# Kernel tuning notes

Measured on AMD Instinct MI355X. Metric: run time of the kernel, lower is better.

## Reference

```python
import jax, jax.numpy as jnp
import numpy as np

IMAGE_SIZE = 224
FMAP_H = FMAP_W = 26   # resnet18 layer2 (28x28) after AvgPool2d(3, stride=1)
N_REWEIGHT = 3
SIGMA = 4.0
KSIZE = 2 * int(4.0 * SIGMA + 0.5) + 1  # 33, kornia-style default kernel for sigma=4


def _gaussian_kernel1d():
    x = np.arange(KSIZE, dtype=np.float64) - (KSIZE - 1) / 2.0
    k = np.exp(-0.5 * (x / SIGMA) ** 2)
    return jnp.asarray((k / k.sum()).astype(np.float32))


def _cdist(x, y):
    # Euclidean cdist: x [N,D], y [M,D] -> [N,M], via the expanded quadratic form.
    x2 = jnp.sum(x * x, axis=1, keepdims=True)          # [N,1]
    y2 = jnp.sum(y * y, axis=1)                          # [M]
    d2 = x2 + y2 - 2.0 * (x @ y.T)                       # [N,M]
    return jnp.sqrt(jnp.maximum(d2, 0.0))


def _gaussian_blur(img):
    # Separable depthwise gaussian blur with reflect padding, img [1,1,H,W].
    k1d = _gaussian_kernel1d()
    pad = (KSIZE - 1) // 2
    x = jnp.pad(img, ((0, 0), (0, 0), (pad, pad), (pad, pad)), mode='reflect')
    kh = k1d.reshape(1, 1, KSIZE, 1)
    kw = k1d.reshape(1, 1, 1, KSIZE)
    dn = ('NCHW', 'OIHW', 'NCHW')
    x = jax.lax.conv_general_dilated(x, kh, (1, 1), 'VALID', dimension_numbers=dn)
    x = jax.lax.conv_general_dilated(x, kw, (1, 1), 'VALID', dimension_numbers=dn)
    return x


def setup_inputs() -> dict:
    key = jax.random.key(0)
    k1, k2 = jax.random.split(key)
    patch = jax.random.normal(k1, (FMAP_H * FMAP_W, 384), dtype=jnp.float32)      # [676, 384]
    patch_lib = jax.random.normal(k2, (100000, 384), dtype=jnp.float32)            # coreset bank
    return {"patch": patch, "patch_lib": patch_lib}


def reference(patch, patch_lib):
    # dist = torch.cdist(patch, patch_lib); min over memory bank
    dist = _cdist(patch, patch_lib)                      # [N, M]
    min_val = jnp.min(dist, axis=1)                      # [N]
    min_idx = jnp.argmin(dist, axis=1)                   # [N]
    s_idx = jnp.argmax(min_val)                          # most anomalous patch
    s_star = min_val[s_idx]
    m_test = patch[s_idx]                                # [D]
    m_star = patch_lib[min_idx[s_idx]]                   # [D]
    # reweighting: k nearest neighbors of m_star in the bank (smallest distances)
    w_dist = jnp.linalg.norm(m_star[None, :] - patch_lib, axis=1)   # [M]
    _, nn_idx = jax.lax.top_k(-w_dist, N_REWEIGHT)                  # indices of k smallest
    m_star_knn = jnp.linalg.norm(m_test[None, :] - patch_lib[nn_idx[1:]], axis=1)  # [k-1]
    D = jnp.sqrt(jnp.asarray(patch.shape[1], dtype=jnp.float32))
    w = 1.0 - jnp.exp(s_star / D) / jnp.sum(jnp.exp(m_star_knn / D))
    s = w * s_star
    # segmentation map: reshape, bilinear upsample (align_corners=False), gaussian blur
    s_map = min_val.reshape(1, 1, FMAP_H, FMAP_W)
    s_map = jax.image.resize(s_map, (1, 1, IMAGE_SIZE, IMAGE_SIZE), method='bilinear')
    s_map = _gaussian_blur(s_map)
    return s, s_map
```

## Files before the change

### kernel.cpp

```cpp
#include <hip/hip_runtime.h>

#define M_PATCH 676
#define K_DIM   384
#define N_LIB   100000
#define BM      128
#define BN      128
#define BK      32
#define LDT     40
#define NCH     782
#define MTILES  6
#define M_PAD   (MTILES*BM)
#define N_PAD   (NCH*BN)
#define NTOPB   1563
#define NCAND   (NTOPB*3)
#define IMG     224
#define FMAP    26
#define KS      33
#define KHALF   16

typedef __attribute__((ext_vector_type(4))) float  f32x4;
typedef __attribute__((ext_vector_type(8))) short  short8;
typedef unsigned long long ull;

static __device__ __forceinline__ unsigned short f2bf(float f) {
  unsigned u = __float_as_uint(f);
  u = u + 0x7FFFu + ((u >> 16) & 1u);
  return (unsigned short)(u >> 16);
}

static __device__ __forceinline__ ull shfl_xor_u64(ull v, int m) {
  unsigned lo = (unsigned)v, hi = (unsigned)(v >> 32);
  lo = __shfl_xor(lo, m, 64);
  hi = __shfl_xor(hi, m, 64);
  return ((ull)hi << 32) | lo;
}

static __device__ __forceinline__ ull umin64(ull a, ull b) { return a < b ? a : b; }
static __device__ __forceinline__ ull umax64(ull a, ull b) { return a > b ? a : b; }

static __device__ __forceinline__ void gld16(const unsigned short* g, unsigned short* l) {
  __builtin_amdgcn_global_load_lds(
      (const __attribute__((address_space(1))) void*)g,
      (__attribute__((address_space(3))) void*)l, 16, 0, 0);
}

__global__ void pc_norms_cvt_kernel(const float* __restrict__ patch, const float* __restrict__ lib,
                                    float* __restrict__ y2, float* __restrict__ x2,
                                    unsigned short* __restrict__ Abf, unsigned short* __restrict__ Bbf,
                                    int do_cvt) {
  const int w = threadIdx.x >> 6, lane = threadIdx.x & 63;
  const long r = (long)blockIdx.x * 4 + w;
  if (r < N_PAD) {
    float s;
    if (r < N_LIB) {
      const float* p = lib + r * K_DIM;
      float v[6];
      s = 0.f;
      #pragma unroll
      for (int j = 0; j < 6; ++j) { v[j] = p[lane + 64 * j]; s += v[j] * v[j]; }
      if (do_cvt) {
        #pragma unroll
        for (int j = 0; j < 6; ++j) Bbf[r * K_DIM + lane + 64 * j] = f2bf(v[j]);
      }
      #pragma unroll
      for (int m = 1; m < 64; m <<= 1) s += __shfl_xor(s, m, 64);
    } else {
      s = __builtin_inff();
      if (do_cvt) {
        #pragma unroll
        for (int j = 0; j < 6; ++j) Bbf[r * K_DIM + lane + 64 * j] = 0;
      }
    }
    if (lane == 0) y2[r] = s;
  } else {
    const long pr = r - N_PAD;
    if (pr < M_PATCH) {
      const float* p = patch + pr * K_DIM;
      float v[6]; float s = 0.f;
      #pragma unroll
      for (int j = 0; j < 6; ++j) { v[j] = p[lane + 64 * j]; s += v[j] * v[j]; }
      if (do_cvt) {
        #pragma unroll
        for (int j = 0; j < 6; ++j) Abf[pr * K_DIM + lane + 64 * j] = f2bf(v[j]);
      }
      #pragma unroll
      for (int m = 1; m < 64; m <<= 1) s += __shfl_xor(s, m, 64);
      if (lane == 0) x2[pr] = s;
    } else if (pr < M_PAD) {
      if (do_cvt) {
        #pragma unroll
        for (int j = 0; j < 6; ++j) Abf[pr * K_DIM + lane + 64 * j] = 0;
      }
    }
  }
}

__launch_bounds__(256, 4)
__global__ void pc_gemm_min_bf16_kernel(const unsigned short* __restrict__ Abf,
                                        const unsigned short* __restrict__ Bbf,
                                        const float* __restrict__ x2g, const float* __restrict__ y2g,
                                        ull* __restrict__ partial) {
  __shared__ unsigned short As[BM * 32];
  __shared__ unsigned short Bs[BN * 32];
  __shared__ float x2s[BM];
  __shared__ float y2s[BN];
  __shared__ ull red[BM * 2];

  const int t = threadIdx.x;
  const int m0 = blockIdx.x * BM;
  const int n0 = blockIdx.y * BN;
  const int wid = t >> 6, lane = t & 63;

  if (t < BM) {
    const int gm = m0 + t;
    x2s[t] = (gm < M_PATCH) ? x2g[gm] : 0.f;
    y2s[t] = y2g[n0 + t];
  }

  const int srow   = (wid << 4) + (lane >> 2);
  const int spiece = (lane & 3) ^ ((lane >> 4) & 3);
  const unsigned short* gA0 = Abf + (size_t)(m0 + srow) * K_DIM + spiece * 8;
  const unsigned short* gA1 = gA0 + (size_t)64 * K_DIM;
  const unsigned short* gB0 = Bbf + (size_t)(n0 + srow) * K_DIM + spiece * 8;
  const unsigned short* gB1 = gB0 + (size_t)64 * K_DIM;
  unsigned short* lA0 = &As[wid * 512];
  unsigned short* lA1 = &As[(wid + 4) * 512];
  unsigned short* lB0 = &Bs[wid * 512];
  unsigned short* lB1 = &Bs[(wid + 4) * 512];

  f32x4 acc[4][4];
  #pragma unroll
  for (int i = 0; i < 4; ++i)
    #pragma unroll
    for (int j = 0; j < 4; ++j) acc[i][j] = (f32x4){0.f, 0.f, 0.f, 0.f};

  const int wm = wid >> 1, wn = wid & 1;
  const int quad = lane >> 4, l15 = lane & 15;
  const int poff = (quad ^ ((l15 >> 2) & 3)) * 8;

  for (int ks = 0; ks < K_DIM / BK; ++ks) {
    __syncthreads();
    gld16(gA0 + ks * BK, lA0);
    gld16(gA1 + ks * BK, lA1);
    gld16(gB0 + ks * BK, lB0);
    gld16(gB1 + ks * BK, lB1);
    __builtin_amdgcn_s_waitcnt(0);
    __syncthreads();

    short8 af[4], bf[4];
    #pragma unroll
    for (int mi = 0; mi < 4; ++mi)
      af[mi] = *(const short8*)&As[(wm * 64 + mi * 16 + l15) * 32 + poff];
    #pragma unroll
    for (int ni = 0; ni < 4; ++ni)
      bf[ni] = *(const short8*)&Bs[(wn * 64 + ni * 16 + l15) * 32 + poff];

    #pragma unroll
    for (int mi = 0; mi < 4; ++mi)
      #pragma unroll
      for (int ni = 0; ni < 4; ++ni)
        acc[mi][ni] = __builtin_amdgcn_mfma_f32_16x16x32_bf16(af[mi], bf[ni], acc[mi][ni], 0, 0, 0);
  }

  #pragma unroll
  for (int mi = 0; mi < 4; ++mi) {
    #pragma unroll
    for (int r = 0; r < 4; ++r) {
      const int row_l = wm * 64 + mi * 16 + quad * 4 + r;
      const float xs = x2s[row_l];
      ull kmin = ~0ull;
      #pragma unroll
      for (int ni = 0; ni < 4; ++ni) {
        const int col_l = wn * 64 + ni * 16 + l15;
        float d2 = xs + y2s[col_l] - 2.0f * acc[mi][ni][r];
        d2 = fmaxf(d2, 0.0f);
        const ull key = ((ull)__float_as_uint(d2) << 32) | (unsigned)(n0 + col_l);
        kmin = umin64(kmin, key);
      }
      #pragma unroll
      for (int off = 1; off < 16; off <<= 1) kmin = umin64(kmin, shfl_xor_u64(kmin, off));
      if (l15 == 0) red[row_l * 2 + wn] = kmin;
    }
  }
  __syncthreads();
  if (t < BM) {
    const ull k = umin64(red[t * 2], red[t * 2 + 1]);
    partial[(size_t)(m0 + t) * NCH + blockIdx.y] = k;
  }
}

__launch_bounds__(256, 2)
__global__ void pc_gemm_min_f32_kernel(const float* __restrict__ A, const float* __restrict__ B,
                                       const float* __restrict__ x2g, const float* __restrict__ y2g,
                                       ull* __restrict__ partial) {
  __shared__ union SMem {
    struct { short As[BM * LDT]; short Bs[BN * LDT]; } st;
    ull red[BM * 32];
  } sm;
  __shared__ float x2s[BM];
  __shared__ float y2s[BN];

  const int t  = threadIdx.x;
  const int m0 = blockIdx.x * BM;
  const int n0 = blockIdx.y * BN;

  if (t < BM) {
    const int gm = m0 + t;
    x2s[t] = (gm < M_PATCH) ? x2g[gm] : 0.f;
    y2s[t] = y2g[n0 + t];
  }

  const int c4 = t & 7;
  const int br = t >> 3;

  const float* pA[4]; const float* pB[4];
  int vA[4], vB[4];
  #pragma unroll
  for (int j = 0; j < 4; ++j) {
    const int row = br + 32 * j;
    const int gm = m0 + row, gn = n0 + row;
    vA[j] = (gm < M_PATCH);
    vB[j] = (gn < N_LIB);
    pA[j] = A + (long)gm * K_DIM + c4 * 4;
    pB[j] = B + (long)gn * K_DIM + c4 * 4;
  }

  f32x4 acc[4][4];
  #pragma unroll
  for (int i = 0; i < 4; ++i)
    #pragma unroll
    for (int j = 0; j < 4; ++j) acc[i][j] = (f32x4){0.f, 0.f, 0.f, 0.f};

  const int wid  = t >> 6;
  const int lane = t & 63;
  const int wm = wid >> 1, wn = wid & 1;
  const int quad = lane >> 4;
  const int l15  = lane & 15;

  for (int ks = 0; ks < K_DIM / BK; ++ks) {
    const int koff = ks * BK;
    __syncthreads();
    #pragma unroll
    for (int j = 0; j < 4; ++j) {
      float4 v = make_float4(0.f, 0.f, 0.f, 0.f);
      if (vA[j]) v = *(const float4*)(pA[j] + koff);
      ushort4 h = make_ushort4(f2bf(v.x), f2bf(v.y), f2bf(v.z), f2bf(v.w));
      *(ushort4*)(&sm.st.As[(br + 32 * j) * LDT + c4 * 4]) = h;
    }
    #pragma unroll
    for (int j = 0; j < 4; ++j) {
      float4 v = make_float4(0.f, 0.f, 0.f, 0.f);
      if (vB[j]) v = *(const float4*)(pB[j] + koff);
      ushort4 h = make_ushort4(f2bf(v.x), f2bf(v.y), f2bf(v.z), f2bf(v.w));
      *(ushort4*)(&sm.st.Bs[(br + 32 * j) * LDT + c4 * 4]) = h;
    }
    __syncthreads();

    short8 af[4], bf[4];
    #pragma unroll
    for (int mi = 0; mi < 4; ++mi)
      af[mi] = *(const short8*)(&sm.st.As[(wm * 64 + mi * 16 + l15) * LDT + quad * 8]);
    #pragma unroll
    for (int ni = 0; ni < 4; ++ni)
      bf[ni] = *(const short8*)(&sm.st.Bs[(wn * 64 + ni * 16 + l15) * LDT + quad * 8]);

    #pragma unroll
    for (int mi = 0; mi < 4; ++mi)
      #pragma unroll
      for (int ni = 0; ni < 4; ++ni)
        acc[mi][ni] = __builtin_amdgcn_mfma_f32_16x16x32_bf16(af[mi], bf[ni], acc[mi][ni], 0, 0, 0);
  }

  __syncthreads();

  #pragma unroll
  for (int mi = 0; mi < 4; ++mi) {
    #pragma unroll
    for (int r = 0; r < 4; ++r) {
      const int row_l = wm * 64 + mi * 16 + quad * 4 + r;
      const float xs = x2s[row_l];
      ull kmin = ~0ull;
      #pragma unroll
      for (int ni = 0; ni < 4; ++ni) {
        const int col_l = wn * 64 + ni * 16 + l15;
        float d2 = xs + y2s[col_l] - 2.0f * acc[mi][ni][r];
        d2 = fmaxf(d2, 0.0f);
        const ull key = ((ull)__float_as_uint(d2) << 32) | (unsigned)(n0 + col_l);
        kmin = umin64(kmin, key);
      }
      sm.red[row_l * 32 + wn * 16 + l15] = kmin;
    }
  }
  __syncthreads();
  if (t < BM) {
    ull k = ~0ull;
    #pragma unroll 8
    for (int c = 0; c < 32; ++c) k = umin64(k, sm.red[t * 32 + c]);
    partial[(long)(m0 + t) * NCH + blockIdx.y] = k;
  }
}

__global__ void pc_reduce_kernel(const ull* __restrict__ partial,
                                 float* __restrict__ minval, unsigned* __restrict__ minidx) {
  const int m = blockIdx.x;
  const int t = threadIdx.x;
  ull k = ~0ull;
  for (int c = t; c < NCH; c += 128) k = umin64(k, partial[(long)m * NCH + c]);
  #pragma unroll
  for (int off = 1; off < 64; off <<= 1) k = umin64(k, shfl_xor_u64(k, off));
  __shared__ ull sh[2];
  if ((t & 63) == 0) sh[t >> 6] = k;
  __syncthreads();
  if (t == 0) {
    k = umin64(sh[0], sh[1]);
    const float d2 = __uint_as_float((unsigned)(k >> 32));
    minval[m] = sqrtf(fmaxf(d2, 0.f));
    minidx[m] = (unsigned)k;
  }
}

__global__ void pc_select_kernel(const float* __restrict__ minval, const unsigned* __restrict__ minidx,
                                 unsigned* __restrict__ scal) {
  const int t = threadIdx.x;
  ull k = 0ull;
  for (int m = t; m < M_PATCH; m += 256) {
    const ull key = ((ull)__float_as_uint(minval[m]) << 32) | (0xFFFFFFFFu - (unsigned)m);
    k = umax64(k, key);
  }
  #pragma unroll
  for (int off = 1; off < 64; off <<= 1) k = umax64(k, shfl_xor_u64(k, off));
  __shared__ ull sh[4];
  if ((t & 63) == 0) sh[t >> 6] = k;
  __syncthreads();
  if (t == 0) {
    #pragma unroll
    for (int w = 1; w < 4; ++w) k = umax64(k, sh[w]);
    const unsigned m = 0xFFFFFFFFu - (unsigned)k;
    scal[0] = m;
    scal[1] = (unsigned)(k >> 32);
    scal[2] = minidx[m];
  }
}

__global__ void pc_wdist_top3_kernel(const float* __restrict__ lib, const unsigned* __restrict__ scal,
                                     ull* __restrict__ cand) {
  __shared__ ull keys[64];
  const int t = threadIdx.x, w = t >> 6, lane = t & 63;
  const float* ms = lib + (size_t)scal[2] * K_DIM;
  float msv[6];
  #pragma unroll
  for (int j = 0; j < 6; ++j) msv[j] = ms[lane + 64 * j];
  const long r0 = (long)blockIdx.x * 64 + w * 16;
  for (int i = 0; i < 16; ++i) {
    const long r = r0 + i;
    ull key = ~0ull;
    if (r < N_LIB) {
      const float* p = lib + r * K_DIM;
      float s = 0.f;
      #pragma unroll
      for (int j = 0; j < 6; ++j) { const float d = p[lane + 64 * j] - msv[j]; s += d * d; }
      #pragma unroll
      for (int m = 1; m < 64; m <<= 1) s += __shfl_xor(s, m, 64);
      key = ((ull)__float_as_uint(s) << 32) | (unsigned)r;
    }
    if (lane == 0) keys[w * 16 + i] = key;
  }
  __syncthreads();
  if (t == 0) {
    ull picks[3];
    #pragma unroll
    for (int p = 0; p < 3; ++p) {
      ull best = ~0ull;
      for (int i = 0; i < 64; ++i) {
        const ull k = keys[i];
        if ((p > 0 && k == picks[0]) || (p > 1 && k == picks[1])) continue;
        best = umin64(best, k);
      }
      picks[p] = best;
      cand[(long)blockIdx.x * 3 + p] = best;
    }
  }
}

__global__ void pc_top3_merge_kernel(const ull* __restrict__ cand, unsigned* __restrict__ scal) {
  __shared__ ull shm[16];
  __shared__ ull picks_s[3];
  const int t = threadIdx.x;
  for (int p = 0; p < 3; ++p) {
    const ull e0 = (p > 0) ? picks_s[0] : 0ull;
    const ull e1 = (p > 1) ? picks_s[1] : 0ull;
    ull k = ~0ull;
    for (int n = t; n < NCAND; n += 1024) {
      const ull c = cand[n];
      if ((p > 0 && c == e0) || (p > 1 && c == e1)) continue;
      k = umin64(k, c);
    }
    #pragma unroll
    for (int off = 1; off < 64; off <<= 1) k = umin64(k, shfl_xor_u64(k, off));
    if ((t & 63) == 0) shm[t >> 6] = k;
    __syncthreads();
    if (t == 0) {
      #pragma unroll
      for (int w = 1; w < 16; ++w) k = umin64(k, shm[w]);
      picks_s[p] = k;
    }
    __syncthreads();
  }
  if (t == 0) { scal[3] = (unsigned)picks_s[1]; scal[4] = (unsigned)picks_s[2]; }
}

__global__ void pc_final_kernel(const float* __restrict__ patch, const float* __restrict__ lib,
                                const unsigned* __restrict__ scal, float* __restrict__ out) {
  const int w = threadIdx.x >> 6, lane = threadIdx.x & 63;
  __shared__ float sh[2];
  const unsigned nn = scal[3 + w];
  const float* mt = patch + (long)scal[0] * K_DIM;
  const float* pv = lib + (long)nn * K_DIM;
  float s = 0.f;
  #pragma unroll
  for (int j = 0; j < 6; ++j) { const float d = mt[lane + 64 * j] - pv[lane + 64 * j]; s += d * d; }
  #pragma unroll
  for (int m = 1; m < 64; m <<= 1) s += __shfl_xor(s, m, 64);
  if (lane == 0) sh[w] = s;
  __syncthreads();
  if (threadIdx.x == 0) {
    const float D = sqrtf((float)K_DIM);
    const float s_star = __uint_as_float(scal[1]);
    const float a = sqrtf(sh[0]), b = sqrtf(sh[1]);
    const float wgt = 1.f - expf(s_star / D) / (expf(a / D) + expf(b / D));
    out[0] = wgt * s_star;
  }
}

__global__ void pc_upsample_kernel(const float* __restrict__ mv, float* __restrict__ up) {
  const int idx = blockIdx.x * 256 + threadIdx.x;
  if (idx >= IMG * IMG) return;
  const int y = idx / IMG, x = idx - y * IMG;
  const float scale = (float)FMAP / (float)IMG;
  const float fy = ((float)y + 0.5f) * scale - 0.5f;
  const float fx = ((float)x + 0.5f) * scale - 0.5f;
  const int iy0 = (int)floorf(fy); const float ty = fy - (float)iy0;
  const int ix0 = (int)floorf(fx); const float tx = fx - (float)ix0;
  const int y0 = min(max(iy0, 0), FMAP - 1), y1 = min(max(iy0 + 1, 0), FMAP - 1);
  const int x0 = min(max(ix0, 0), FMAP - 1), x1 = min(max(ix0 + 1, 0), FMAP - 1);
  const float v00 = mv[y0 * FMAP + x0], v01 = mv[y0 * FMAP + x1];
  const float v10 = mv[y1 * FMAP + x0], v11 = mv[y1 * FMAP + x1];
  const float v0 = v00 + (v01 - v00) * tx;
  const float v1 = v10 + (v11 - v10) * tx;
  up[idx] = v0 + (v1 - v0) * ty;
}

static __device__ __forceinline__ int pc_refl(int i) {
  return i < 0 ? -i : (i >= IMG ? 2 * IMG - 2 - i : i);
}

__global__ void pc_blur_kernel(const float* __restrict__ src, float* __restrict__ dst, int along_x) {
  __shared__ double kd[KS];
  __shared__ double ksum;
  __shared__ float kf[KS];
  const int t = threadIdx.x;
  if (t < KS) { const double xx = (double)(t - KHALF) / 4.0; kd[t] = exp(-0.5 * xx * xx); }
  __syncthreads();
  if (t == 0) { double s = 0.0; for (int i = 0; i < KS; ++i) s += kd[i]; ksum = s; }
  __syncthreads();
  if (t < KS) kf[t] = (float)(kd[t] / ksum);
  __syncthreads();
  const int idx = blockIdx.x * 256 + t;
  if (idx >= IMG * IMG) return;
  const int y = idx / IMG, x = idx - y * IMG;
  float s = 0.f;
  if (along_x) {
    #pragma unroll
    for (int i = 0; i < KS; ++i) s += kf[i] * src[y * IMG + pc_refl(x + i - KHALF)];
  } else {
    #pragma unroll
    for (int i = 0; i < KS; ++i) s += kf[i] * src[pc_refl(y + i - KHALF) * IMG + x];
  }
  dst[idx] = s;
}

extern "C" void kernel_launch(void* const* d_in, const int* in_sizes, int n_in,
                              void* d_out, int out_size, void* d_ws, size_t ws_size,
                              hipStream_t stream) {
  const float* patch = (const float*)d_in[0];
  const float* lib   = (const float*)d_in[1];
  float* out = (float*)d_out;

  char* p = (char*)d_ws;
  auto take = [&](size_t n) { char* q = p; p += (n + 511) & ~(size_t)511; return q; };
  float* y2        = (float*)take((size_t)N_PAD * 4);
  float* x2        = (float*)take((size_t)M_PAD * 4);
  ull* partial     = (ull*)take((size_t)M_PAD * NCH * 8);
  float* minval    = (float*)take((size_t)M_PATCH * 4);
  unsigned* minidx = (unsigned*)take((size_t)M_PATCH * 4);
  unsigned* scal   = (unsigned*)take(64);
  ull* cand        = (ull*)take((size_t)NCAND * 8);
  float* up        = (float*)take((size_t)IMG * IMG * 4);
  float* tmpb      = (float*)take((size_t)IMG * IMG * 4);
  unsigned short* Abf = (unsigned short*)take((size_t)M_PAD * K_DIM * 2);
  unsigned short* Bbf = (unsigned short*)take((size_t)N_PAD * K_DIM * 2);
  const int use_bf16 = ((size_t)(p - (char*)d_ws) <= ws_size);
  (void)in_sizes; (void)n_in; (void)out_size;

  const int norm_rows = N_PAD + M_PAD;
  pc_norms_cvt_kernel<<<(norm_rows + 3) / 4, 256, 0, stream>>>(patch, lib, y2, x2, Abf, Bbf, use_bf16);

  dim3 g(MTILES, NCH);
  if (use_bf16)
    pc_gemm_min_bf16_kernel<<<g, 256, 0, stream>>>(Abf, Bbf, x2, y2, partial);
  else
    pc_gemm_min_f32_kernel<<<g, 256, 0, stream>>>(patch, lib, x2, y2, partial);

  pc_reduce_kernel<<<M_PATCH, 128, 0, stream>>>(partial, minval, minidx);
  pc_select_kernel<<<1, 256, 0, stream>>>(minval, minidx, scal);
  pc_wdist_top3_kernel<<<NTOPB, 256, 0, stream>>>(lib, scal, cand);
  pc_top3_merge_kernel<<<1, 1024, 0, stream>>>(cand, scal);
  pc_final_kernel<<<1, 128, 0, stream>>>(patch, lib, scal, out);

  pc_upsample_kernel<<<(IMG * IMG + 255) / 256, 256, 0, stream>>>(minval, up);
  pc_blur_kernel<<<(IMG * IMG + 255) / 256, 256, 0, stream>>>(up, tmpb, 0);
  pc_blur_kernel<<<(IMG * IMG + 255) / 256, 256, 0, stream>>>(tmpb, out + 1, 1);
}
```

Before: 390.9 us.

## Remap GEMM blocks per XCD, stage K=64 per sync, vectorize loads

The GEMM grid becomes 1D with an XCD-aware mapping, so each XCD handles a contiguous range of library chunks and all six M tiles of a chunk stay on the same XCD. This is meant to improve L2 reuse of B tiles. The K loop now loads two 32-wide slices per barrier pair, halving synchronisations at the cost of more LDS per block. The partial buffer is transposed to chunk-major for coalesced writes, and the f32 fallback GEMM and workspace-size check are removed. The norm and wdist kernels switch to float2 loads and stores.

```diff
diff --git a/kernel.cpp b/kernel.cpp
--- a/kernel.cpp
+++ b/kernel.cpp
@@ -5,12 +5,12 @@
 #define N_LIB   100000
 #define BM      128
 #define BN      128
-#define BK      32
-#define LDT     40
 #define NCH     782
 #define MTILES  6
 #define M_PAD   (MTILES*BM)
 #define N_PAD   (NCH*BN)
+#define XCHUNK  98
+#define GRID_GEMM (8*XCHUNK*MTILES)
 #define NTOPB   1563
 #define NCAND   (NTOPB*3)
 #define IMG     224
@@ -46,51 +46,46 @@
 
 __global__ void pc_norms_cvt_kernel(const float* __restrict__ patch, const float* __restrict__ lib,
                                     float* __restrict__ y2, float* __restrict__ x2,
-                                    unsigned short* __restrict__ Abf, unsigned short* __restrict__ Bbf,
-                                    int do_cvt) {
+                                    unsigned short* __restrict__ Abf, unsigned short* __restrict__ Bbf) {
   const int w = threadIdx.x >> 6, lane = threadIdx.x & 63;
   const long r = (long)blockIdx.x * 4 + w;
   if (r < N_PAD) {
     float s;
     if (r < N_LIB) {
-      const float* p = lib + r * K_DIM;
-      float v[6];
+      const float2* p = (const float2*)(lib + r * K_DIM);
+      ushort2* q = (ushort2*)(Bbf + r * K_DIM);
+      float2 v[3];
       s = 0.f;
       #pragma unroll
-      for (int j = 0; j < 6; ++j) { v[j] = p[lane + 64 * j]; s += v[j] * v[j]; }
-      if (do_cvt) {
-        #pragma unroll
-        for (int j = 0; j < 6; ++j) Bbf[r * K_DIM + lane + 64 * j] = f2bf(v[j]);
-      }
+      for (int j = 0; j < 3; ++j) { v[j] = p[lane + 64 * j]; s += v[j].x * v[j].x + v[j].y * v[j].y; }
+      #pragma unroll
+      for (int j = 0; j < 3; ++j) q[lane + 64 * j] = make_ushort2(f2bf(v[j].x), f2bf(v[j].y));
       #pragma unroll
       for (int m = 1; m < 64; m <<= 1) s += __shfl_xor(s, m, 64);
     } else {
       s = __builtin_inff();
-      if (do_cvt) {
-        #pragma unroll
-        for (int j = 0; j < 6; ++j) Bbf[r * K_DIM + lane + 64 * j] = 0;
-      }
+      ushort2* q = (ushort2*)(Bbf + r * K_DIM);
+      #pragma unroll
+      for (int j = 0; j < 3; ++j) q[lane + 64 * j] = make_ushort2(0, 0);
     }
     if (lane == 0) y2[r] = s;
   } else {
     const long pr = r - N_PAD;
     if (pr < M_PATCH) {
-      const float* p = patch + pr * K_DIM;
-      float v[6]; float s = 0.f;
-      #pragma unroll
-      for (int j = 0; j < 6; ++j) { v[j] = p[lane + 64 * j]; s += v[j] * v[j]; }
-      if (do_cvt) {
-        #pragma unroll
-        for (int j = 0; j < 6; ++j) Abf[pr * K_DIM + lane + 64 * j] = f2bf(v[j]);
-      }
+      const float2* p = (const float2*)(patch + pr * K_DIM);
+      ushort2* q = (ushort2*)(Abf + pr * K_DIM);
+      float2 v[3]; float s = 0.f;
+      #pragma unroll
+      for (int j = 0; j < 3; ++j) { v[j] = p[lane + 64 * j]; s += v[j].x * v[j].x + v[j].y * v[j].y; }
+      #pragma unroll
+      for (int j = 0; j < 3; ++j) q[lane + 64 * j] = make_ushort2(f2bf(v[j].x), f2bf(v[j].y));
       #pragma unroll
       for (int m = 1; m < 64; m <<= 1) s += __shfl_xor(s, m, 64);
       if (lane == 0) x2[pr] = s;
     } else if (pr < M_PAD) {
-      if (do_cvt) {
-        #pragma unroll
-        for (int j = 0; j < 6; ++j) Abf[pr * K_DIM + lane + 64 * j] = 0;
-      }
+      ushort2* q = (ushort2*)(Abf + pr * K_DIM);
+      #pragma unroll
+      for (int j = 0; j < 3; ++j) q[lane + 64 * j] = make_ushort2(0, 0);
     }
   }
 }
@@ -100,15 +95,21 @@
                                         const unsigned short* __restrict__ Bbf,
                                         const float* __restrict__ x2g, const float* __restrict__ y2g,
                                         ull* __restrict__ partial) {
-  __shared__ unsigned short As[BM * 32];
-  __shared__ unsigned short Bs[BN * 32];
+  __shared__ unsigned short As[2][BM * 32];
+  __shared__ unsigned short Bs[2][BN * 32];
   __shared__ float x2s[BM];
   __shared__ float y2s[BN];
   __shared__ ull red[BM * 2];
 
+  const int l = blockIdx.x;
+  const int xcd = l & 7, slot = l >> 3;
+  const int chunk = xcd * XCHUNK + slot / MTILES;
+  const int mtile = slot % MTILES;
+  if (chunk >= NCH) return;
+
   const int t = threadIdx.x;
-  const int m0 = blockIdx.x * BM;
-  const int n0 = blockIdx.y * BN;
+  const int m0 = mtile * BM;
+  const int n0 = chunk * BN;
   const int wid = t >> 6, lane = t & 63;
 
   if (t < BM) {
@@ -123,10 +124,6 @@
   const unsigned short* gA1 = gA0 + (size_t)64 * K_DIM;
   const unsigned short* gB0 = Bbf + (size_t)(n0 + srow) * K_DIM + spiece * 8;
   const unsigned short* gB1 = gB0 + (size_t)64 * K_DIM;
-  unsigned short* lA0 = &As[wid * 512];
-  unsigned short* lA1 = &As[(wid + 4) * 512];
-  unsigned short* lB0 = &Bs[wid * 512];
-  unsigned short* lB1 = &Bs[(wid + 4) * 512];
 
   f32x4 acc[4][4];
   #pragma unroll
@@ -138,28 +135,34 @@
   const int quad = lane >> 4, l15 = lane & 15;
   const int poff = (quad ^ ((l15 >> 2) & 3)) * 8;
 
-  for (int ks = 0; ks < K_DIM / BK; ++ks) {
+  for (int ks = 0; ks < K_DIM / 64; ++ks) {
     __syncthreads();
-    gld16(gA0 + ks * BK, lA0);
-    gld16(gA1 + ks * BK, lA1);
-    gld16(gB0 + ks * BK, lB0);
-    gld16(gB1 + ks * BK, lB1);
+    #pragma unroll
+    for (int h = 0; h < 2; ++h) {
+      const int ko = ks * 64 + h * 32;
+      gld16(gA0 + ko, &As[h][wid * 512]);
+      gld16(gA1 + ko, &As[h][(wid + 4) * 512]);
+      gld16(gB0 + ko, &Bs[h][wid * 512]);
+      gld16(gB1 + ko, &Bs[h][(wid + 4) * 512]);
+    }
     __builtin_amdgcn_s_waitcnt(0);
     __syncthreads();
 
-    short8 af[4], bf[4];
-    #pragma unroll
-    for (int mi = 0; mi < 4; ++mi)
-      af[mi] = *(const short8*)&As[(wm * 64 + mi * 16 + l15) * 32 + poff];
-    #pragma unroll
-    for (int ni = 0; ni < 4; ++ni)
-      bf[ni] = *(const short8*)&Bs[(wn * 64 + ni * 16 + l15) * 32 + poff];
-
-    #pragma unroll
-    for (int mi = 0; mi < 4; ++mi)
+    #pragma unroll
+    for (int h = 0; h < 2; ++h) {
+      short8 af[4], bf[4];
+      #pragma unroll
+      for (int mi = 0; mi < 4; ++mi)
+        af[mi] = *(const short8*)&As[h][(wm * 64 + mi * 16 + l15) * 32 + poff];
       #pragma unroll
       for (int ni = 0; ni < 4; ++ni)
-        acc[mi][ni] = __builtin_amdgcn_mfma_f32_16x16x32_bf16(af[mi], bf[ni], acc[mi][ni], 0, 0, 0);
+        bf[ni] = *(const short8*)&Bs[h][(wn * 64 + ni * 16 + l15) * 32 + poff];
+      #pragma unroll
+      for (int mi = 0; mi < 4; ++mi)
+        #pragma unroll
+        for (int ni = 0; ni < 4; ++ni)
+          acc[mi][ni] = __builtin_amdgcn_mfma_f32_16x16x32_bf16(af[mi], bf[ni], acc[mi][ni], 0, 0, 0);
+    }
   }
 
   #pragma unroll
@@ -185,118 +188,7 @@
   __syncthreads();
   if (t < BM) {
     const ull k = umin64(red[t * 2], red[t * 2 + 1]);
-    partial[(size_t)(m0 + t) * NCH + blockIdx.y] = k;
-  }
-}
-
-__launch_bounds__(256, 2)
-__global__ void pc_gemm_min_f32_kernel(const float* __restrict__ A, const float* __restrict__ B,
-                                       const float* __restrict__ x2g, const float* __restrict__ y2g,
-                                       ull* __restrict__ partial) {
-  __shared__ union SMem {
-    struct { short As[BM * LDT]; short Bs[BN * LDT]; } st;
-    ull red[BM * 32];
-  } sm;
-  __shared__ float x2s[BM];
-  __shared__ float y2s[BN];
-
-  const int t  = threadIdx.x;
-  const int m0 = blockIdx.x * BM;
-  const int n0 = blockIdx.y * BN;
-
-  if (t < BM) {
-    const int gm = m0 + t;
-    x2s[t] = (gm < M_PATCH) ? x2g[gm] : 0.f;
-    y2s[t] = y2g[n0 + t];
-  }
-
-  const int c4 = t & 7;
-  const int br = t >> 3;
-
-  const float* pA[4]; const float* pB[4];
-  int vA[4], vB[4];
-  #pragma unroll
-  for (int j = 0; j < 4; ++j) {
-    const int row = br + 32 * j;
-    const int gm = m0 + row, gn = n0 + row;
-    vA[j] = (gm < M_PATCH);
-    vB[j] = (gn < N_LIB);
-    pA[j] = A + (long)gm * K_DIM + c4 * 4;
-    pB[j] = B + (long)gn * K_DIM + c4 * 4;
-  }
-
-  f32x4 acc[4][4];
-  #pragma unroll
-  for (int i = 0; i < 4; ++i)
-    #pragma unroll
-    for (int j = 0; j < 4; ++j) acc[i][j] = (f32x4){0.f, 0.f, 0.f, 0.f};
-
-  const int wid  = t >> 6;
-  const int lane = t & 63;
-  const int wm = wid >> 1, wn = wid & 1;
-  const int quad = lane >> 4;
-  const int l15  = lane & 15;
-
-  for (int ks = 0; ks < K_DIM / BK; ++ks) {
-    const int koff = ks * BK;
-    __syncthreads();
-    #pragma unroll
-    for (int j = 0; j < 4; ++j) {
-      float4 v = make_float4(0.f, 0.f, 0.f, 0.f);
-      if (vA[j]) v = *(const float4*)(pA[j] + koff);
-      ushort4 h = make_ushort4(f2bf(v.x), f2bf(v.y), f2bf(v.z), f2bf(v.w));
-      *(ushort4*)(&sm.st.As[(br + 32 * j) * LDT + c4 * 4]) = h;
-    }
-    #pragma unroll
-    for (int j = 0; j < 4; ++j) {
-      float4 v = make_float4(0.f, 0.f, 0.f, 0.f);
-      if (vB[j]) v = *(const float4*)(pB[j] + koff);
-      ushort4 h = make_ushort4(f2bf(v.x), f2bf(v.y), f2bf(v.z), f2bf(v.w));
-      *(ushort4*)(&sm.st.Bs[(br + 32 * j) * LDT + c4 * 4]) = h;
-    }
-    __syncthreads();
-
-    short8 af[4], bf[4];
-    #pragma unroll
-    for (int mi = 0; mi < 4; ++mi)
-      af[mi] = *(const short8*)(&sm.st.As[(wm * 64 + mi * 16 + l15) * LDT + quad * 8]);
-    #pragma unroll
-    for (int ni = 0; ni < 4; ++ni)
-      bf[ni] = *(const short8*)(&sm.st.Bs[(wn * 64 + ni * 16 + l15) * LDT + quad * 8]);
-
-    #pragma unroll
-    for (int mi = 0; mi < 4; ++mi)
-      #pragma unroll
-      for (int ni = 0; ni < 4; ++ni)
-        acc[mi][ni] = __builtin_amdgcn_mfma_f32_16x16x32_bf16(af[mi], bf[ni], acc[mi][ni], 0, 0, 0);
-  }
-
-  __syncthreads();
-
-  #pragma unroll
-  for (int mi = 0; mi < 4; ++mi) {
-    #pragma unroll
-    for (int r = 0; r < 4; ++r) {
-      const int row_l = wm * 64 + mi * 16 + quad * 4 + r;
-      const float xs = x2s[row_l];
-      ull kmin = ~0ull;
-      #pragma unroll
-      for (int ni = 0; ni < 4; ++ni) {
-        const int col_l = wn * 64 + ni * 16 + l15;
-        float d2 = xs + y2s[col_l] - 2.0f * acc[mi][ni][r];
-        d2 = fmaxf(d2, 0.0f);
-        const ull key = ((ull)__float_as_uint(d2) << 32) | (unsigned)(n0 + col_l);
-        kmin = umin64(kmin, key);
-      }
-      sm.red[row_l * 32 + wn * 16 + l15] = kmin;
-    }
-  }
-  __syncthreads();
-  if (t < BM) {
-    ull k = ~0ull;
-    #pragma unroll 8
-    for (int c = 0; c < 32; ++c) k = umin64(k, sm.red[t * 32 + c]);
-    partial[(long)(m0 + t) * NCH + blockIdx.y] = k;
+    partial[(size_t)chunk * M_PAD + m0 + t] = k;
   }
 }
 
@@ -305,7 +197,7 @@
   const int m = blockIdx.x;
   const int t = threadIdx.x;
   ull k = ~0ull;
-  for (int c = t; c < NCH; c += 128) k = umin64(k, partial[(long)m * NCH + c]);
+  for (int c = t; c < NCH; c += 128) k = umin64(k, partial[(size_t)c * M_PAD + m]);
   #pragma unroll
   for (int off = 1; off < 64; off <<= 1) k = umin64(k, shfl_xor_u64(k, off));
   __shared__ ull sh[2];
@@ -346,19 +238,23 @@
                                      ull* __restrict__ cand) {
   __shared__ ull keys[64];
   const int t = threadIdx.x, w = t >> 6, lane = t & 63;
-  const float* ms = lib + (size_t)scal[2] * K_DIM;
-  float msv[6];
-  #pragma unroll
-  for (int j = 0; j < 6; ++j) msv[j] = ms[lane + 64 * j];
+  const float2* ms = (const float2*)(lib + (size_t)scal[2] * K_DIM);
+  float2 msv[3];
+  #pragma unroll
+  for (int j = 0; j < 3; ++j) msv[j] = ms[lane + 64 * j];
   const long r0 = (long)blockIdx.x * 64 + w * 16;
   for (int i = 0; i < 16; ++i) {
     const long r = r0 + i;
     ull key = ~0ull;
     if (r < N_LIB) {
-      const float* p = lib + r * K_DIM;
+      const float2* p = (const float2*)(lib + r * K_DIM);
       float s = 0.f;
       #pragma unroll
-      for (int j = 0; j < 6; ++j) { const float d = p[lane + 64 * j] - msv[j]; s += d * d; }
+      for (int j = 0; j < 3; ++j) {
+        const float2 v = p[lane + 64 * j];
+        const float dx = v.x - msv[j].x, dy = v.y - msv[j].y;
+        s += dx * dx + dy * dy;
+      }
       #pragma unroll
       for (int m = 1; m < 64; m <<= 1) s += __shfl_xor(s, m, 64);
       key = ((ull)__float_as_uint(s) << 32) | (unsigned)r;
@@ -490,7 +386,7 @@
   auto take = [&](size_t n) { char* q = p; p += (n + 511) & ~(size_t)511; return q; };
   float* y2        = (float*)take((size_t)N_PAD * 4);
   float* x2        = (float*)take((size_t)M_PAD * 4);
-  ull* partial     = (ull*)take((size_t)M_PAD * NCH * 8);
+  ull* partial     = (ull*)take((size_t)NCH * M_PAD * 8);
   float* minval    = (float*)take((size_t)M_PATCH * 4);
   unsigned* minidx = (unsigned*)take((size_t)M_PATCH * 4);
   unsigned* scal   = (unsigned*)take(64);
@@ -499,17 +395,12 @@
   float* tmpb      = (float*)take((size_t)IMG * IMG * 4);
   unsigned short* Abf = (unsigned short*)take((size_t)M_PAD * K_DIM * 2);
   unsigned short* Bbf = (unsigned short*)take((size_t)N_PAD * K_DIM * 2);
-  const int use_bf16 = ((size_t)(p - (char*)d_ws) <= ws_size);
-  (void)in_sizes; (void)n_in; (void)out_size;
+  (void)in_sizes; (void)n_in; (void)out_size; (void)ws_size;
 
   const int norm_rows = N_PAD + M_PAD;
-  pc_norms_cvt_kernel<<<(norm_rows + 3) / 4, 256, 0, stream>>>(patch, lib, y2, x2, Abf, Bbf, use_bf16);
-
-  dim3 g(MTILES, NCH);
-  if (use_bf16)
-    pc_gemm_min_bf16_kernel<<<g, 256, 0, stream>>>(Abf, Bbf, x2, y2, partial);
-  else
-    pc_gemm_min_f32_kernel<<<g, 256, 0, stream>>>(patch, lib, x2, y2, partial);
+  pc_norms_cvt_kernel<<<(norm_rows + 3) / 4, 256, 0, stream>>>(patch, lib, y2, x2, Abf, Bbf);
+
+  pc_gemm_min_bf16_kernel<<<GRID_GEMM, 256, 0, stream>>>(Abf, Bbf, x2, y2, partial);
 
   pc_reduce_kernel<<<M_PATCH, 128, 0, stream>>>(partial, minval, minidx);
   pc_select_kernel<<<1, 256, 0, stream>>>(minval, minidx, scal);
```

Measured after the change: 386.8 us. About the same (-1.1%).
